# Kernel optimization log

Hardware: AMD Instinct MI355X
Metric: run time of the kernel (lower is better)

## Reference

```python
import jax, jax.numpy as jnp
import numpy as np

S, B, H, V = 512, 512, 256, 128


def setup_inputs() -> dict:
    key = jax.random.key(0)
    ks = jax.random.split(key, 11)
    sd = 0.05
    return {
        "x": jax.random.randint(ks[0], (S, B), 0, V, dtype=jnp.int32),
        "w_ih0": jax.random.normal(ks[1], (4 * H, 1), jnp.float32) * sd,
        "w_hh0": jax.random.normal(ks[2], (4 * H, H), jnp.float32) * sd,
        "b_ih0": jax.random.normal(ks[3], (4 * H,), jnp.float32) * sd,
        "b_hh0": jax.random.normal(ks[4], (4 * H,), jnp.float32) * sd,
        "w_ih1": jax.random.normal(ks[5], (4 * H, H), jnp.float32) * sd,
        "w_hh1": jax.random.normal(ks[6], (4 * H, H), jnp.float32) * sd,
        "b_ih1": jax.random.normal(ks[7], (4 * H,), jnp.float32) * sd,
        "b_hh1": jax.random.normal(ks[8], (4 * H,), jnp.float32) * sd,
        "W_out": jax.random.normal(ks[9], (V, H), jnp.float32) * sd,
        "b_out": jax.random.normal(ks[10], (V,), jnp.float32) * sd,
    }


def _lstm_cell(x_t, h, c, w_ih, w_hh, b_ih, b_hh):
    # PyTorch gate order: i, f, g, o
    gates = x_t @ w_ih.T + h @ w_hh.T + b_ih + b_hh  # [B, 4H]
    i, f, g, o = jnp.split(gates, 4, axis=-1)
    c_new = jax.nn.sigmoid(f) * c + jax.nn.sigmoid(i) * jnp.tanh(g)
    h_new = jax.nn.sigmoid(o) * jnp.tanh(c_new)
    return h_new, c_new


def reference(x, w_ih0, w_hh0, b_ih0, b_hh0, w_ih1, w_hh1, b_ih1, b_hh1, W_out, b_out):
    s, b = x.shape
    xf = x.astype(jnp.float32)[..., None]  # [S, B, 1] raw token ids as floats

    def step(carry, x_t):
        h0, c0, h1, c1 = carry
        h0, c0 = _lstm_cell(x_t, h0, c0, w_ih0, w_hh0, b_ih0, b_hh0)
        h1, c1 = _lstm_cell(h0, h1, c1, w_ih1, w_hh1, b_ih1, b_hh1)
        return (h0, c0, h1, c1), h1

    z = jnp.zeros((b, w_hh0.shape[1]), jnp.float32)
    _, hs = jax.lax.scan(step, (z, z, z, z), xf)  # hs: [S, B, H]
    return hs @ W_out.T + b_out  # [S, B, V]
```

## Files before the change

### kernel.cpp

```cpp
#include <hip/hip_runtime.h>


#define S_ 512
#define B_ 512
#define H_ 256
#define V_ 128

typedef _Float16 f16;
typedef __attribute__((ext_vector_type(8))) _Float16 f16x8;
typedef __attribute__((ext_vector_type(4))) float f32x4;
typedef unsigned long long u64;
typedef unsigned u32;
typedef unsigned short u16;

#define OFF_B0   0
#define OFF_B1   524288
#define OFF_BP   1572864
#define OFF_EX   1638400
#define OFF_TAG  2686976

__device__ __forceinline__ float sigm(float z) { return 1.0f / (1.0f + __expf(-z)); }
__device__ __forceinline__ float tanh_fast(float z) {
  return 2.0f / (1.0f + __expf(-2.0f * z)) - 1.0f;
}

__global__ void prep_kernel(const float* __restrict__ w_hh0,
                            const float* __restrict__ w_ih1, const float* __restrict__ w_hh1,
                            const float* __restrict__ W_out, void* __restrict__ ws) {
  int idx = blockIdx.x * blockDim.x + threadIdx.x;
  f16* wsh = (f16*)ws;
  if (idx < 32768) {
    int j = idx >> 12, w = (idx >> 9) & 7, kk = (idx >> 6) & 7, lane = idx & 63;
    int gate = w >> 1, half = w & 1;
    int hcol = j * 32 + half * 16 + (lane & 15);
    int G = gate * H_ + hcol;
    int k0 = kk * 32 + (lane >> 4) * 8;
    f16x8 v;
    #pragma unroll
    for (int i = 0; i < 8; ++i) v[i] = (f16)w_hh0[G * H_ + k0 + i];
    *(f16x8*)(wsh + idx * 8) = v;
  } else if (idx < 32768 + 65536) {
    int t = idx - 32768;
    int j = t >> 13, w = (t >> 10) & 7, kk = (t >> 6) & 15, lane = t & 63;
    int gate = w >> 1, half = w & 1;
    int hcol = j * 32 + half * 16 + (lane & 15);
    int G = gate * H_ + hcol;
    int k0 = kk * 32 + (lane >> 4) * 8;
    const float* src = (k0 < H_) ? (w_ih1 + G * H_ + k0) : (w_hh1 + G * H_ + (k0 - H_));
    f16x8 v;
    #pragma unroll
    for (int i = 0; i < 8; ++i) v[i] = (f16)src[i];
    *(f16x8*)(wsh + 262144 + t * 8) = v;
  } else if (idx < 32768 + 65536 + 4096) {
    int t = idx - (32768 + 65536);
    int j = t >> 9, w = (t >> 6) & 7, lane = t & 63;
    int vcol = j * 16 + (lane & 15);
    int k0 = w * 32 + (lane >> 4) * 8;
    f16x8 v;
    #pragma unroll
    for (int i = 0; i < 8; ++i) v[i] = (f16)W_out[vcol * H_ + k0 + i];
    *(f16x8*)(wsh + 786432 + t * 8) = v;
  } else if (idx < 32768 + 65536 + 4096 + 8192) {
    ((u32*)((char*)ws + OFF_TAG))[idx - 102400] = 0u;
  }
}

__device__ __forceinline__ u64 aload64(const u64* p) {
  return __hip_atomic_load((u64*)p, __ATOMIC_RELAXED, __HIP_MEMORY_SCOPE_AGENT);
}
__device__ __forceinline__ u32 aload32(const u32* p) {
  return __hip_atomic_load((u32*)p, __ATOMIC_RELAXED, __HIP_MEMORY_SCOPE_AGENT);
}
__device__ __forceinline__ void astore32(u32* p, u32 v) {
  __hip_atomic_store(p, v, __ATOMIC_RELAXED, __HIP_MEMORY_SCOPE_AGENT);
}
__device__ __forceinline__ void astore16(u16* p, u16 v) {
  __hip_atomic_store(p, v, __ATOMIC_RELAXED, __HIP_MEMORY_SCOPE_AGENT);
}

__device__ __forceinline__ f16x8 afrag(const f16* buf, int lane, int kk) {
  return *(const f16x8*)(buf + kk * 512 + lane * 8);
}

__global__ __launch_bounds__(512, 2) void lstm_r10(const int* __restrict__ x,
                                                   const f16* __restrict__ wts,
                                                   char* __restrict__ ex,
                                                   u32* __restrict__ tags,
                                                   const float* __restrict__ w_ih0,
                                                   const float* __restrict__ b_ih0,
                                                   const float* __restrict__ b_hh0,
                                                   const float* __restrict__ b_ih1,
                                                   const float* __restrict__ b_hh1,
                                                   const float* __restrict__ b_out,
                                                   float* __restrict__ out) {
  __shared__ __align__(16) f16 H0[4096], H1[4096];
  __shared__ __align__(16) float gsc0[4][16][33];
  __shared__ __align__(16) float gsc1[4][16][33];
  __shared__ __align__(16) float ppart[4][8][64];

  const int tid  = threadIdx.x;
  const int lane = tid & 63;
  const int w    = tid >> 6;
  const int bg   = blockIdx.x >> 3;
  const int j    = blockIdx.x & 7;

  f16x8 B0r[8], B1r[16], BPr;
  {
    const f16* p0 = wts + (size_t)(j * 8 + w) * 8 * 512 + lane * 8;
    #pragma unroll
    for (int kk = 0; kk < 8; ++kk) B0r[kk] = *(const f16x8*)(p0 + kk * 512);
    const f16* p1 = wts + 262144 + (size_t)(j * 8 + w) * 16 * 512 + lane * 8;
    #pragma unroll
    for (int kk = 0; kk < 16; ++kk) B1r[kk] = *(const f16x8*)(p1 + kk * 512);
    BPr = *(const f16x8*)(wts + 786432 + (size_t)(j * 8 + w) * 512 + lane * 8);
  }

  const int erow = tid >> 5, ecol = tid & 31;
  const int hcol = j * 32 + ecol;
  const int browg = bg * 16 + erow;
  float wxv[4], bz0v[4], bz1v[4];
  #pragma unroll
  for (int g = 0; g < 4; ++g) {
    int G = g * H_ + hcol;
    wxv[g]  = w_ih0[G];
    bz0v[g] = b_ih0[G] + b_hh0[G];
    bz1v[g] = b_ih1[G] + b_hh1[G];
  }
  const float bo = (tid < 256) ? b_out[j * 16 + (tid & 15)] : 0.f;

  char* exG = ex + (size_t)bg * 32768;
  u32* tagB = tags + (size_t)bg * 8 * 32;
  u32* myTag = tagB + j * 32;
  u32* peerTag = tagB + w * 32;

  const int grow = lane & 15;
  const int gbyte = grow * 512 + w * 64 + ((lane >> 4) << 4);

  float c0 = 0.f, c1 = 0.f;

  ((u64*)H0)[tid] = 0ull; ((u64*)H0)[tid + 512] = 0ull;
  ((u64*)H1)[tid] = 0ull; ((u64*)H1)[tid + 512] = 0ull;
  __syncthreads();

  #pragma unroll 1
  for (int t = 0; t <= S_ + 1; ++t) {
    float xf = (t < S_) ? (float)x[t * B_ + browg] : 0.f;

    if (t > 0) {
      const u32 need = (u32)t;
      while (aload32(peerTag) < need) __builtin_amdgcn_s_sleep(1);
      asm volatile("" ::: "memory");
      const char* slotR = exG + ((t - 1) & 1) * 16384;
      u64 q0 = aload64((const u64*)(slotR + gbyte));
      u64 q1 = aload64((const u64*)(slotR + gbyte) + 1);
      u64 q2 = aload64((const u64*)(slotR + 8192 + gbyte));
      u64 q3 = aload64((const u64*)(slotR + 8192 + gbyte) + 1);
      ((u64*)H0)[tid * 2]     = q0;
      ((u64*)H0)[tid * 2 + 1] = q1;
      ((u64*)H1)[tid * 2]     = q2;
      ((u64*)H1)[tid * 2 + 1] = q3;
    }
    __syncthreads();

    {
      f32x4 acc0 = {0.f, 0.f, 0.f, 0.f};
      f32x4 acc1 = {0.f, 0.f, 0.f, 0.f};
      f32x4 ap   = {0.f, 0.f, 0.f, 0.f};
      #pragma unroll
      for (int kk = 0; kk < 8; ++kk) {
        f16x8 ah = afrag(H0, lane, kk);
        acc0 = __builtin_amdgcn_mfma_f32_16x16x32_f16(ah, B0r[kk], acc0, 0, 0, 0);
        acc1 = __builtin_amdgcn_mfma_f32_16x16x32_f16(ah, B1r[kk], acc1, 0, 0, 0);
      }
      #pragma unroll
      for (int kk = 0; kk < 8; ++kk) {
        f16x8 ah = afrag(H1, lane, kk);
        acc1 = __builtin_amdgcn_mfma_f32_16x16x32_f16(ah, B1r[kk + 8], acc1, 0, 0, 0);
      }
      ap = __builtin_amdgcn_mfma_f32_16x16x32_f16(afrag(H1, lane, w), BPr, ap, 0, 0, 0);
      const int gate = w >> 1, half = w & 1;
      const int c16 = lane & 15, r0 = (lane >> 4) * 4;
      #pragma unroll
      for (int r = 0; r < 4; ++r) {
        gsc0[gate][r0 + r][half * 16 + c16] = acc0[r];
        gsc1[gate][r0 + r][half * 16 + c16] = acc1[r];
        ppart[r][w][lane] = ap[r];
      }
    }
    __syncthreads();

    u16* slotW = (u16*)(exG + (t & 1) * 16384);
    if (t < S_) {
      float gi = gsc0[0][erow][ecol] + xf * wxv[0] + bz0v[0];
      float gf = gsc0[1][erow][ecol] + xf * wxv[1] + bz0v[1];
      float gg = gsc0[2][erow][ecol] + xf * wxv[2] + bz0v[2];
      float go = gsc0[3][erow][ecol] + xf * wxv[3] + bz0v[3];
      c0 = sigm(gf) * c0 + sigm(gi) * tanh_fast(gg);
      float h0 = sigm(go) * tanh_fast(c0);
      union { f16 h; u16 u; } hb; hb.h = (f16)h0;
      astore16(slotW + erow * 256 + hcol, hb.u);
    }
    if (t <= S_) {
      float h1 = 0.f;
      if (t >= 1) {
        float gi = gsc1[0][erow][ecol] + bz1v[0];
        float gf = gsc1[1][erow][ecol] + bz1v[1];
        float gg = gsc1[2][erow][ecol] + bz1v[2];
        float go = gsc1[3][erow][ecol] + bz1v[3];
        c1 = sigm(gf) * c1 + sigm(gi) * tanh_fast(gg);
        h1 = sigm(go) * tanh_fast(c1);
      }
      union { f16 h; u16 u; } hb; hb.h = (f16)h1;
      astore16(slotW + 4096 + erow * 256 + hcol, hb.u);
    }
    if (t >= 2 && tid < 256) {
      int prow = tid >> 4, pvc = tid & 15;
      int plane = (prow >> 2) * 16 + pvc, preg = prow & 3;
      float s = bo;
      #pragma unroll
      for (int ww = 0; ww < 8; ++ww) s += ppart[preg][ww][plane];
      out[((size_t)((t - 2) * B_ + bg * 16 + prow)) * V_ + j * 16 + pvc] = s;
    }

    if (t <= S_) {
      asm volatile("s_waitcnt vmcnt(0)" ::: "memory");
      __syncthreads();
      if (tid == 0) astore32(myTag, (u32)(t + 1));
    }
  }
}

extern "C" void kernel_launch(void* const* d_in, const int* in_sizes, int n_in,
                              void* d_out, int out_size, void* d_ws, size_t ws_size,
                              hipStream_t stream) {
  const int*   x     = (const int*)d_in[0];
  const float* w_ih0 = (const float*)d_in[1];
  const float* w_hh0 = (const float*)d_in[2];
  const float* b_ih0 = (const float*)d_in[3];
  const float* b_hh0 = (const float*)d_in[4];
  const float* w_ih1 = (const float*)d_in[5];
  const float* w_hh1 = (const float*)d_in[6];
  const float* b_ih1 = (const float*)d_in[7];
  const float* b_hh1 = (const float*)d_in[8];
  const float* W_out = (const float*)d_in[9];
  const float* b_out = (const float*)d_in[10];

  prep_kernel<<<432, 256, 0, stream>>>(w_hh0, w_ih1, w_hh1, W_out, d_ws);

  lstm_r10<<<256, 512, 0, stream>>>(x, (const f16*)d_ws,
                                    (char*)d_ws + OFF_EX, (u32*)((char*)d_ws + OFF_TAG),
                                    w_ih0, b_ih0, b_hh0, b_ih1, b_hh1, b_out,
                                    (float*)d_out);
}
```

Before: 1.911 ms.

## Replace per-block tag flags with stamped data words for inter-block sync

Drops the separate tag counters and the end-of-step waitcnt/barrier/flag store. Each exchanged fp16 hidden value is now written as a 32-bit word whose upper half carries the step stamp, and readers poll the data words themselves until every stamp matches before packing the values into shared memory. This removes a barrier and a flag round trip from every timestep's critical path. In exchange the exchange buffer doubles in size, reads carry twice the bytes, and the prep kernel must zero the larger buffer.

Result: slower. 2.052 ms (+7.4%).

```diff
diff --git a/kernel.cpp b/kernel.cpp
--- a/kernel.cpp
+++ b/kernel.cpp
@@ -17,7 +17,6 @@
 #define OFF_B1   524288
 #define OFF_BP   1572864
 #define OFF_EX   1638400
-#define OFF_TAG  2686976
 
 __device__ __forceinline__ float sigm(float z) { return 1.0f / (1.0f + __expf(-z)); }
 __device__ __forceinline__ float tanh_fast(float z) {
@@ -60,32 +59,29 @@
     #pragma unroll
     for (int i = 0; i < 8; ++i) v[i] = (f16)W_out[vcol * H_ + k0 + i];
     *(f16x8*)(wsh + 786432 + t * 8) = v;
-  } else if (idx < 32768 + 65536 + 4096 + 8192) {
-    ((u32*)((char*)ws + OFF_TAG))[idx - 102400] = 0u;
+  } else if (idx < 102400 + 262144) {
+    ((u64*)((char*)ws + OFF_EX))[idx - 102400] = 0ull;
   }
 }
 
 __device__ __forceinline__ u64 aload64(const u64* p) {
   return __hip_atomic_load((u64*)p, __ATOMIC_RELAXED, __HIP_MEMORY_SCOPE_AGENT);
 }
-__device__ __forceinline__ u32 aload32(const u32* p) {
-  return __hip_atomic_load((u32*)p, __ATOMIC_RELAXED, __HIP_MEMORY_SCOPE_AGENT);
-}
 __device__ __forceinline__ void astore32(u32* p, u32 v) {
   __hip_atomic_store(p, v, __ATOMIC_RELAXED, __HIP_MEMORY_SCOPE_AGENT);
 }
-__device__ __forceinline__ void astore16(u16* p, u16 v) {
-  __hip_atomic_store(p, v, __ATOMIC_RELAXED, __HIP_MEMORY_SCOPE_AGENT);
+
+__device__ __forceinline__ u32 pack2(u64 q) {
+  return (u32)(q & 0xffffu) | (((u32)(q >> 32)) << 16);
 }
 
 __device__ __forceinline__ f16x8 afrag(const f16* buf, int lane, int kk) {
   return *(const f16x8*)(buf + kk * 512 + lane * 8);
 }
 
-__global__ __launch_bounds__(512, 2) void lstm_r10(const int* __restrict__ x,
+__global__ __launch_bounds__(512, 2) void lstm_r11(const int* __restrict__ x,
                                                    const f16* __restrict__ wts,
-                                                   char* __restrict__ ex,
-                                                   u32* __restrict__ tags,
+                                                   u32* __restrict__ ex,
                                                    const float* __restrict__ w_ih0,
                                                    const float* __restrict__ b_ih0,
                                                    const float* __restrict__ b_hh0,
@@ -128,13 +124,11 @@
   }
   const float bo = (tid < 256) ? b_out[j * 16 + (tid & 15)] : 0.f;
 
-  char* exG = ex + (size_t)bg * 32768;
-  u32* tagB = tags + (size_t)bg * 8 * 32;
-  u32* myTag = tagB + j * 32;
-  u32* peerTag = tagB + w * 32;
+  u32* exG = ex + (size_t)bg * 16384;
 
   const int grow = lane & 15;
-  const int gbyte = grow * 512 + w * 64 + ((lane >> 4) << 4);
+  const int gcol = w * 32 + ((lane >> 4) << 3);
+  const int gidx = grow * 256 + gcol;
 
   float c0 = 0.f, c1 = 0.f;
 
@@ -147,18 +141,27 @@
     float xf = (t < S_) ? (float)x[t * B_ + browg] : 0.f;
 
     if (t > 0) {
-      const u32 need = (u32)t;
-      while (aload32(peerTag) < need) __builtin_amdgcn_s_sleep(1);
+      const u32 want = (u32)t & 0xffffu;
+      const u64 pat  = ((u64)want << 16) | ((u64)want << 48);
+      const u64 mask = 0xffff0000ffff0000ull;
+      const u64* p0 = (const u64*)(exG + ((t - 1) & 1) * 8192 + gidx);
+      const u64* p1 = p0 + 2048;
+      u64 a0, a1, a2, a3, b0, b1, b2, b3;
+      for (;;) {
+        a0 = aload64(p0);     a1 = aload64(p0 + 1);
+        a2 = aload64(p0 + 2); a3 = aload64(p0 + 3);
+        b0 = aload64(p1);     b1 = aload64(p1 + 1);
+        b2 = aload64(p1 + 2); b3 = aload64(p1 + 3);
+        u64 bad = (a0 ^ pat) | (a1 ^ pat) | (a2 ^ pat) | (a3 ^ pat)
+                | (b0 ^ pat) | (b1 ^ pat) | (b2 ^ pat) | (b3 ^ pat);
+        if ((bad & mask) == 0) break;
+        __builtin_amdgcn_s_sleep(1);
+      }
       asm volatile("" ::: "memory");
-      const char* slotR = exG + ((t - 1) & 1) * 16384;
-      u64 q0 = aload64((const u64*)(slotR + gbyte));
-      u64 q1 = aload64((const u64*)(slotR + gbyte) + 1);
-      u64 q2 = aload64((const u64*)(slotR + 8192 + gbyte));
-      u64 q3 = aload64((const u64*)(slotR + 8192 + gbyte) + 1);
-      ((u64*)H0)[tid * 2]     = q0;
-      ((u64*)H0)[tid * 2 + 1] = q1;
-      ((u64*)H1)[tid * 2]     = q2;
-      ((u64*)H1)[tid * 2 + 1] = q3;
+      u32* d0 = (u32*)H0 + tid * 4;
+      u32* d1 = (u32*)H1 + tid * 4;
+      d0[0] = pack2(a0); d0[1] = pack2(a1); d0[2] = pack2(a2); d0[3] = pack2(a3);
+      d1[0] = pack2(b0); d1[1] = pack2(b1); d1[2] = pack2(b2); d1[3] = pack2(b3);
     }
     __syncthreads();
 
@@ -189,16 +192,21 @@
     }
     __syncthreads();
 
-    u16* slotW = (u16*)(exG + (t & 1) * 16384);
-    if (t < S_) {
-      float gi = gsc0[0][erow][ecol] + xf * wxv[0] + bz0v[0];
-      float gf = gsc0[1][erow][ecol] + xf * wxv[1] + bz0v[1];
-      float gg = gsc0[2][erow][ecol] + xf * wxv[2] + bz0v[2];
-      float go = gsc0[3][erow][ecol] + xf * wxv[3] + bz0v[3];
-      c0 = sigm(gf) * c0 + sigm(gi) * tanh_fast(gg);
-      float h0 = sigm(go) * tanh_fast(c0);
-      union { f16 h; u16 u; } hb; hb.h = (f16)h0;
-      astore16(slotW + erow * 256 + hcol, hb.u);
+    u32* slotW = exG + (t & 1) * 8192;
+    const u32 stamp = ((u32)(t + 1) & 0xffffu) << 16;
+    if (t <= S_) {
+      u32 word = stamp;
+      if (t < S_) {
+        float gi = gsc0[0][erow][ecol] + xf * wxv[0] + bz0v[0];
+        float gf = gsc0[1][erow][ecol] + xf * wxv[1] + bz0v[1];
+        float gg = gsc0[2][erow][ecol] + xf * wxv[2] + bz0v[2];
+        float go = gsc0[3][erow][ecol] + xf * wxv[3] + bz0v[3];
+        c0 = sigm(gf) * c0 + sigm(gi) * tanh_fast(gg);
+        float h0 = sigm(go) * tanh_fast(c0);
+        union { f16 h; u16 u; } hb; hb.h = (f16)h0;
+        word |= (u32)hb.u;
+      }
+      astore32(slotW + erow * 256 + hcol, word);
     }
     if (t <= S_) {
       float h1 = 0.f;
@@ -211,7 +219,7 @@
         h1 = sigm(go) * tanh_fast(c1);
       }
       union { f16 h; u16 u; } hb; hb.h = (f16)h1;
-      astore16(slotW + 4096 + erow * 256 + hcol, hb.u);
+      astore32(slotW + 4096 + erow * 256 + hcol, stamp | (u32)hb.u);
     }
     if (t >= 2 && tid < 256) {
       int prow = tid >> 4, pvc = tid & 15;
@@ -220,12 +228,6 @@
       #pragma unroll
       for (int ww = 0; ww < 8; ++ww) s += ppart[preg][ww][plane];
       out[((size_t)((t - 2) * B_ + bg * 16 + prow)) * V_ + j * 16 + pvc] = s;
-    }
-
-    if (t <= S_) {
-      asm volatile("s_waitcnt vmcnt(0)" ::: "memory");
-      __syncthreads();
-      if (tid == 0) astore32(myTag, (u32)(t + 1));
     }
   }
 }
@@ -245,10 +247,10 @@
   const float* W_out = (const float*)d_in[9];
   const float* b_out = (const float*)d_in[10];
 
-  prep_kernel<<<432, 256, 0, stream>>>(w_hh0, w_ih1, w_hh1, W_out, d_ws);
-
-  lstm_r10<<<256, 512, 0, stream>>>(x, (const f16*)d_ws,
-                                    (char*)d_ws + OFF_EX, (u32*)((char*)d_ws + OFF_TAG),
+  prep_kernel<<<1424, 256, 0, stream>>>(w_hh0, w_ih1, w_hh1, W_out, d_ws);
+
+  lstm_r11<<<256, 512, 0, stream>>>(x, (const f16*)d_ws,
+                                    (u32*)((char*)d_ws + OFF_EX),
                                     w_ih0, b_ih0, b_hh0, b_ih1, b_hh1, b_out,
                                     (float*)d_out);
 }
```
